# Optimization experiments

Hardware: AMD Instinct MI355X
Metric: run time of the kernel (lower is better)

## Reference

```python
import jax, jax.numpy as jnp
import numpy as np

B, T, D, H = 32, 512, 1024, 1024


def setup_inputs() -> dict:
    key = jax.random.key(0)
    k1, k2, k3 = jax.random.split(key, 3)
    x = jax.random.normal(k1, (B, T, D), dtype=jnp.float32)
    c0 = jnp.zeros((B, H), dtype=jnp.float32)
    h0 = jnp.zeros((B, H), dtype=jnp.float32)
    # scale weights so gates do not saturate
    Wx = jax.random.normal(k2, (D, 4 * H), dtype=jnp.float32) * 0.05
    Wh = jax.random.normal(k3, (H, 4 * H), dtype=jnp.float32) * 0.05
    b = jnp.zeros((4 * H,), dtype=jnp.float32)
    return {"x": x, "c0": c0, "h0": h0, "Wx": Wx, "Wh": Wh, "b": b}


def reference(x, c0, h0, Wx, Wh, b):
    # Flax LSTMCell: gates = x @ Wx + h @ Wh + b, split into i,f,g,o.
    # Precompute the input projection for all timesteps (one big GEMM).
    xW = jnp.einsum('btd,dg->btg', x, Wx) + b  # [B,T,4H]

    def step(carry, xw_t):
        c, h = carry
        gates = xw_t + h @ Wh  # [B,4H]
        i, f, g, o = jnp.split(gates, 4, axis=-1)
        i = jax.nn.sigmoid(i)
        f = jax.nn.sigmoid(f)
        g = jnp.tanh(g)
        o = jax.nn.sigmoid(o)
        c_new = f * c + i * g
        h_new = o * jnp.tanh(c_new)
        return (c_new, h_new), h_new

    (cT, hT), ys = jax.lax.scan(step, (c0, h0), jnp.swapaxes(xW, 0, 1))
    outputs = jnp.swapaxes(ys, 0, 1)  # [B,T,H]
    return outputs, (cT, hT)
```

## Files before the change

kernel.cpp:

```cpp
#include <hip/hip_runtime.h>
#include <cstddef>

#define NB 32
#define NT 512
#define ND 1024
#define NH 1024
#define NG 4096
#define GRID 256

typedef unsigned short ushortT;
typedef __attribute__((ext_vector_type(8))) short short8;
typedef __attribute__((ext_vector_type(4))) float f32x4;
typedef __attribute__((ext_vector_type(4))) unsigned uint4v;

#define GLL16(g, l) __builtin_amdgcn_global_load_lds(                      \
    (const __attribute__((address_space(1))) void*)(g),                    \
    (__attribute__((address_space(3))) void*)(l), 16, 0, 0)

__device__ __forceinline__ ushortT f2bf(float f) {
    union { float f; unsigned u; } v; v.f = f;
    unsigned r = v.u + 0x7FFFu + ((v.u >> 16) & 1u);
    return (ushortT)(r >> 16);
}
__device__ __forceinline__ float bf2f(ushortT u) {
    union { unsigned u; float f; } v; v.u = (unsigned)u << 16; return v.f;
}

__device__ __forceinline__ float pick4(float a0, float a1, float a2, float a3, int s) {
    float lo = (s & 1) ? a1 : a0;
    float hi = (s & 1) ? a3 : a2;
    return (s & 2) ? hi : lo;
}

__device__ __forceinline__ float fsigmoid(float x) {
    return __builtin_amdgcn_rcpf(1.f + __expf(-x));
}
__device__ __forceinline__ float ftanh(float x) {
    float xc = fminf(fmaxf(x, -15.f), 15.f);
    float e  = __expf(-2.f * xc);
    return (1.f - e) * __builtin_amdgcn_rcpf(1.f + e);
}

__global__ __launch_bounds__(256) void cast_bf16(const float* __restrict__ src,
                                                 ushortT* __restrict__ dst, int n4)
{
    int i = blockIdx.x * 256 + threadIdx.x;
    if (i < n4) {
        float4 v = ((const float4*)src)[i];
        ushort4 o;
        o.x = f2bf(v.x); o.y = f2bf(v.y); o.z = f2bf(v.z); o.w = f2bf(v.w);
        ((ushort4*)dst)[i] = o;
    }
}

__global__ __launch_bounds__(256) void transpose_cast(
    const float* __restrict__ src, ushortT* __restrict__ dst, int permute)
{
    __shared__ ushortT tile[64][66];
    const int c0 = blockIdx.x * 64, r0 = blockIdx.y * 64;
    const int cc = threadIdx.x & 63, rq = threadIdx.x >> 6;
    #pragma unroll
    for (int ps = 0; ps < 16; ++ps) {
        int r = ps * 4 + rq;
        tile[cc][r] = f2bf(src[(size_t)(r0 + r) * NG + c0 + cc]);
    }
    __syncthreads();
    #pragma unroll
    for (int ps = 0; ps < 16; ++ps) {
        int cl = ps * 4 + rq;
        int n  = c0 + cl;
        int drow = permute ? ((((n & 1023) >> 2) << 4) | ((n >> 10) << 2) | (n & 3))
                           : n;
        dst[(size_t)drow * 1024 + r0 + cc] = tile[cl][cc];
    }
}

__global__ __launch_bounds__(256) void gemm_xw_mfma(
    const ushortT* __restrict__ xb,
    const ushortT* __restrict__ wxT,
    const float* __restrict__ bias,
    ushortT* __restrict__ XWPb,
    int t0, int Tc, int tcsh)
{
    __shared__ ushortT As[128 * 32];
    __shared__ ushortT Bs[128 * 32];

    const int tid  = threadIdx.x;
    const int lane = tid & 63;
    const int wv   = tid >> 6;
    const int wr   = wv >> 1, wc = wv & 1;
    const int n0   = blockIdx.x * 128;
    const int m0   = blockIdx.y * 128;

    const int c1 = tid, c2 = tid + 256;
    const int rm1 = m0 + (c1 >> 2), rm2 = m0 + (c2 >> 2);
    const int xr1 = ((rm1 >> tcsh) * NT) + t0 + (rm1 & (Tc - 1));
    const int xr2 = ((rm2 >> tcsh) * NT) + t0 + (rm2 & (Tc - 1));
    const ushortT* ap1 = xb + (size_t)xr1 * ND + (c1 & 3) * 8;
    const ushortT* ap2 = xb + (size_t)xr2 * ND + (c2 & 3) * 8;
    const ushortT* bp1 = wxT + (size_t)(n0 + (c1 >> 2)) * ND + (c1 & 3) * 8;
    const ushortT* bp2 = wxT + (size_t)(n0 + (c2 >> 2)) * ND + (c2 & 3) * 8;

    f32x4 acc[4][4];
    #pragma unroll
    for (int m = 0; m < 4; ++m)
        #pragma unroll
        for (int n = 0; n < 4; ++n) acc[m][n] = (f32x4){0.f, 0.f, 0.f, 0.f};

    const int arow_base = (wr * 64 + (lane & 15)) * 32 + (lane >> 4) * 8;
    const int brow_base = (wc * 64 + (lane & 15)) * 32 + (lane >> 4) * 8;

    for (int k0 = 0; k0 < ND; k0 += 32) {
        __syncthreads();
        GLL16(ap1 + k0, &As[c1 * 8]);
        GLL16(ap2 + k0, &As[c2 * 8]);
        GLL16(bp1 + k0, &Bs[c1 * 8]);
        GLL16(bp2 + k0, &Bs[c2 * 8]);
        __syncthreads();
        short8 af[4], bf[4];
        #pragma unroll
        for (int m = 0; m < 4; ++m)
            af[m] = *(const short8*)&As[arow_base + m * 16 * 32];
        #pragma unroll
        for (int n = 0; n < 4; ++n)
            bf[n] = *(const short8*)&Bs[brow_base + n * 16 * 32];
        #pragma unroll
        for (int m = 0; m < 4; ++m)
            #pragma unroll
            for (int n = 0; n < 4; ++n)
                acc[m][n] = __builtin_amdgcn_mfma_f32_16x16x32_bf16(
                    af[m], bf[n], acc[m][n], 0, 0, 0);
    }

    #pragma unroll
    for (int n = 0; n < 4; ++n) {
        int col = n0 + wc * 64 + n * 16 + (lane & 15);
        int pc  = (((col & 1023) >> 2) << 4) | ((col >> 10) << 2) | (col & 3);
        float bs = bias[col];
        #pragma unroll
        for (int m = 0; m < 4; ++m) {
            #pragma unroll
            for (int r = 0; r < 4; ++r) {
                int rm = m0 + wr * 64 + m * 16 + (lane >> 4) * 4 + r;
                int b  = rm >> tcsh, tr = rm & (Tc - 1);
                XWPb[((size_t)tr * NB + b) * NG + pc] = f2bf(acc[m][n][r] + bs);
            }
        }
    }
}

__global__ __launch_bounds__(512) void lstm_persist(
    const ushortT* __restrict__ XWPb,
    const ushortT* __restrict__ whpT,
    ushortT* __restrict__ hbuf,
    const float* __restrict__ cinit,
    float* __restrict__ cT,
    float* __restrict__ out,
    float* __restrict__ hT,
    unsigned* __restrict__ flags,
    int t0, int Tc)
{
    __shared__ float red[2][64][16][4];

    const int tid  = threadIdx.x;
    const int lane = tid & 63;
    const int w    = tid >> 6;
    const int grp  = blockIdx.x & 7;
    const int sl   = blockIdx.x >> 3;

    const int lo = lane & 15;
    const int hi = lane >> 4;

    short8 Bf[8][4];
    #pragma unroll
    for (int ct = 0; ct < 8; ++ct)
        #pragma unroll
        for (int ks = 0; ks < 4; ++ks)
            Bf[ct][ks] = *(const short8*)(whpT
                + (size_t)(sl * 128 + ct * 16 + lo) * NH + w * 128 + ks * 32 + hi * 8);

    const int arow = tid >> 7;
    const int acol = tid & 127;
    const int gq   = (acol >> 2) & 3;
    const int u4   = (acol >> 4) * 4 + (acol & 3);
    const int brow = grp * 4 + arow;
    const int j    = sl * 32 + u4;

    float creg = cinit[(size_t)brow * NH + j];

    const int aoff = (grp * 4 + (lane & 3)) * NH + w * 128 + hi * 8;

    unsigned* const fg = flags + grp * 32;
    unsigned* const fpoll = fg + 4 * w + (lane & 3);
    unsigned* const fmine = fg + sl;

    ushortT xvr = XWPb[(size_t)brow * NG + sl * 128 + acol];

    const int tend = t0 + Tc;
    for (int t = t0; t < tend; ++t) {
        const int trel = t - t0;
        const int par  = t & 1;
        const ushortT* hRp = hbuf + (size_t)par * (NB * NH);
        ushortT*       hWp = hbuf + (size_t)(par ^ 1) * (NB * NH);

        if (trel) {
            const unsigned tgt = (unsigned)trel;
            for (int it = 0; it < (1 << 17); ++it) {
                unsigned v = __hip_atomic_load(fpoll, __ATOMIC_RELAXED,
                                               __HIP_MEMORY_SCOPE_AGENT);
                if (__all(v >= tgt)) break;
            }
        }

        const unsigned long long* sp = (const unsigned long long*)(hRp + aoff);
        unsigned long long p0, p1;
        uint4v Araw0, Araw1, Araw2, Araw3;
        p0 = __hip_atomic_load(sp + 0, __ATOMIC_RELAXED, __HIP_MEMORY_SCOPE_AGENT);
        p1 = __hip_atomic_load(sp + 1, __ATOMIC_RELAXED, __HIP_MEMORY_SCOPE_AGENT);
        Araw0 = (uint4v){(unsigned)p0, (unsigned)(p0 >> 32), (unsigned)p1, (unsigned)(p1 >> 32)};
        p0 = __hip_atomic_load(sp + 8, __ATOMIC_RELAXED, __HIP_MEMORY_SCOPE_AGENT);
        p1 = __hip_atomic_load(sp + 9, __ATOMIC_RELAXED, __HIP_MEMORY_SCOPE_AGENT);
        Araw1 = (uint4v){(unsigned)p0, (unsigned)(p0 >> 32), (unsigned)p1, (unsigned)(p1 >> 32)};
        p0 = __hip_atomic_load(sp + 16, __ATOMIC_RELAXED, __HIP_MEMORY_SCOPE_AGENT);
        p1 = __hip_atomic_load(sp + 17, __ATOMIC_RELAXED, __HIP_MEMORY_SCOPE_AGENT);
        Araw2 = (uint4v){(unsigned)p0, (unsigned)(p0 >> 32), (unsigned)p1, (unsigned)(p1 >> 32)};
        p0 = __hip_atomic_load(sp + 24, __ATOMIC_RELAXED, __HIP_MEMORY_SCOPE_AGENT);
        p1 = __hip_atomic_load(sp + 25, __ATOMIC_RELAXED, __HIP_MEMORY_SCOPE_AGENT);
        Araw3 = (uint4v){(unsigned)p0, (unsigned)(p0 >> 32), (unsigned)p1, (unsigned)(p1 >> 32)};

        short8 A0 = *(short8*)&Araw0;
        short8 A1 = *(short8*)&Araw1;
        short8 A2 = *(short8*)&Araw2;
        short8 A3 = *(short8*)&Araw3;

        #pragma unroll
        for (int ct = 0; ct < 8; ++ct) {
            f32x4 a = (f32x4){0.f, 0.f, 0.f, 0.f};
            a = __builtin_amdgcn_mfma_f32_16x16x32_bf16(A0, Bf[ct][0], a, 0, 0, 0);
            a = __builtin_amdgcn_mfma_f32_16x16x32_bf16(A1, Bf[ct][1], a, 0, 0, 0);
            a = __builtin_amdgcn_mfma_f32_16x16x32_bf16(A2, Bf[ct][2], a, 0, 0, 0);
            a = __builtin_amdgcn_mfma_f32_16x16x32_bf16(A3, Bf[ct][3], a, 0, 0, 0);
            if (hi == 0)
                *(f32x4*)&red[par][w * 8 + ct][lo][0] = a;
        }
        __syncthreads();

        float g = bf2f(xvr);
        #pragma unroll
        for (int wv = 0; wv < 8; ++wv)
            g += red[par][wv * 8 + (acol >> 4)][acol & 15][arow];

        float g4  = __shfl_xor(g, 4);
        float g8  = __shfl_xor(g, 8);
        float g12 = __shfl_xor(g, 12);

        float gi = pick4(g, g4, g8, g12, gq);
        float gf = pick4(g, g4, g8, g12, gq ^ 1);
        float gg = pick4(g, g4, g8, g12, gq ^ 2);
        float go = pick4(g, g4, g8, g12, gq ^ 3);

        float iv = fsigmoid(gi);
        float fv = fsigmoid(gf);
        float gv = ftanh(gg);
        float ov = fsigmoid(go);
        float cn = fv * creg + iv * gv;
        float hn = ov * ftanh(cn);
        creg = cn;

        float ph = __shfl_xor(hn, 1);
        const bool wl = (gq == 0) && ((acol & 1) == 0);
        unsigned pair = (unsigned)f2bf(hn) | ((unsigned)f2bf(ph) << 16);
        unsigned* hdst = (unsigned*)(hWp + (size_t)brow * NH + (j & ~1));
        if (wl)
            __hip_atomic_store(hdst, pair, __ATOMIC_RELAXED,
                               __HIP_MEMORY_SCOPE_AGENT);

        asm volatile("s_waitcnt vmcnt(0)" ::: "memory");
        __syncthreads();

        if (t != tend - 1) {
            if (tid == 0)
                __hip_atomic_store(fmine, (unsigned)(trel + 1),
                                   __ATOMIC_RELAXED, __HIP_MEMORY_SCOPE_AGENT);
            if (wl)
                *(float2*)&out[((size_t)brow * NT + t) * NH + j] = make_float2(hn, ph);
            xvr = XWPb[((size_t)(trel + 1) * NB + brow) * NG + sl * 128 + acol];
        } else {
            if (wl)
                *(float2*)&out[((size_t)brow * NT + t) * NH + j] = make_float2(hn, ph);
            if (gq == 0) {
                if (t == NT - 1) hT[(size_t)brow * NH + j] = hn;
                cT[(size_t)brow * NH + j] = cn;
            }
        }
    }
}

extern "C" void kernel_launch(void* const* d_in, const int* in_sizes, int n_in,
                              void* d_out, int out_size, void* d_ws, size_t ws_size,
                              hipStream_t stream) {
    const float* x    = (const float*)d_in[0];
    const float* c0   = (const float*)d_in[1];
    const float* h0   = (const float*)d_in[2];
    const float* Wx   = (const float*)d_in[3];
    const float* Wh   = (const float*)d_in[4];
    const float* bias = (const float*)d_in[5];

    float* out = (float*)d_out;
    float* cT  = out + (size_t)NB * NT * NH;
    float* hT  = cT + (size_t)NB * NH;

    ushortT* xb   = (ushortT*)d_ws;
    ushortT* wxT  = xb  + (size_t)NB * NT * ND;
    ushortT* whpT = wxT + (size_t)NG * ND;
    ushortT* hbuf = whpT + (size_t)NG * NH;
    unsigned* flags = (unsigned*)(hbuf + 2 * NB * NH);
    ushortT* xwpb = (ushortT*)(flags + 8 * 32 + 32);

    const size_t fixed = ((size_t)NB * NT * ND + (size_t)NG * ND + (size_t)NG * NH
                          + 2 * NB * NH) * sizeof(ushortT)
                         + (8 * 32 + 32) * sizeof(unsigned) + 256;
    int Tc = 512;
    while (Tc > 4 && fixed + (size_t)NB * Tc * NG * sizeof(ushortT) > ws_size)
        Tc >>= 1;
    int tcsh = 31 - __builtin_clz(Tc);

    cast_bf16<<<(NB * NT * ND / 4 + 255) / 256, 256, 0, stream>>>(x, xb, NB * NT * ND / 4);
    cast_bf16<<<(NB * NH / 4 + 255) / 256, 256, 0, stream>>>(h0, hbuf, NB * NH / 4);
    transpose_cast<<<dim3(64, 16), 256, 0, stream>>>(Wx, wxT, 0);
    transpose_cast<<<dim3(64, 16), 256, 0, stream>>>(Wh, whpT, 1);

    for (int t0 = 0; t0 < NT; t0 += Tc) {
        dim3 g(NG / 128, (NB * Tc) / 128);
        gemm_xw_mfma<<<g, 256, 0, stream>>>(xb, wxT, bias, xwpb, t0, Tc, tcsh);
        hipMemsetAsync(flags, 0, (8 * 32) * sizeof(unsigned), stream);
        lstm_persist<<<GRID, 512, 0, stream>>>(
            xwpb, whpT, hbuf,
            (t0 == 0) ? c0 : (const float*)cT,
            cT, out, hT, flags, t0, Tc);
    }
}
```

Measured before the change: 2.370 ms.

## Replace per-block flag barrier with step-tagged h words polled directly

Each bf16 pair of h is now stored as a 64-bit word whose upper half carries the timestep tag. Consumers spin on the data words themselves instead of on separate per-block flags. This removes the flag store, the vmcnt wait and the trailing __syncthreads per step, so one global round trip leaves the critical path. In exchange the hidden-state buffer and each poll's traffic double, since 16 u64 atomic loads replace 8. Correctness relies on tags differing between reuses of the double buffer, including across chunk launches.

```diff
diff --git a/kernel.cpp b/kernel.cpp
--- a/kernel.cpp
+++ b/kernel.cpp
@@ -9,6 +9,7 @@
 #define GRID 256
 
 typedef unsigned short ushortT;
+typedef unsigned long long u64;
 typedef __attribute__((ext_vector_type(8))) short short8;
 typedef __attribute__((ext_vector_type(4))) float f32x4;
 typedef __attribute__((ext_vector_type(4))) unsigned uint4v;
@@ -51,6 +52,16 @@
         o.x = f2bf(v.x); o.y = f2bf(v.y); o.z = f2bf(v.z); o.w = f2bf(v.w);
         ((ushort4*)dst)[i] = o;
     }
+}
+
+__global__ __launch_bounds__(256) void cast_h0_tagged(
+    const float* __restrict__ h0, u64* __restrict__ dst)
+{
+    int i = blockIdx.x * 256 + threadIdx.x;
+    int row = i >> 9, p = i & 511;
+    unsigned pair = (unsigned)f2bf(h0[(size_t)row * NH + 2 * p])
+                  | ((unsigned)f2bf(h0[(size_t)row * NH + 2 * p + 1]) << 16);
+    dst[i] = (u64)pair;
 }
 
 __global__ __launch_bounds__(256) void transpose_cast(
@@ -152,12 +163,11 @@
 __global__ __launch_bounds__(512) void lstm_persist(
     const ushortT* __restrict__ XWPb,
     const ushortT* __restrict__ whpT,
-    ushortT* __restrict__ hbuf,
+    u64* __restrict__ hbuf64,
     const float* __restrict__ cinit,
     float* __restrict__ cT,
     float* __restrict__ out,
     float* __restrict__ hT,
-    unsigned* __restrict__ flags,
     int t0, int Tc)
 {
     __shared__ float red[2][64][16][4];
@@ -188,11 +198,9 @@
 
     float creg = cinit[(size_t)brow * NH + j];
 
-    const int aoff = (grp * 4 + (lane & 3)) * NH + w * 128 + hi * 8;
-
-    unsigned* const fg = flags + grp * 32;
-    unsigned* const fpoll = fg + 4 * w + (lane & 3);
-    unsigned* const fmine = fg + sl;
+    const int prow = grp * 4 + (lane & 3);
+    const size_t pbase = (size_t)prow * 512 + w * 64 + hi * 4;
+    const size_t wbase = (size_t)brow * 512 + sl * 16 + (u4 >> 1);
 
     ushortT xvr = XWPb[(size_t)brow * NG + sl * 128 + acol];
 
@@ -200,38 +208,46 @@
     for (int t = t0; t < tend; ++t) {
         const int trel = t - t0;
         const int par  = t & 1;
-        const ushortT* hRp = hbuf + (size_t)par * (NB * NH);
-        ushortT*       hWp = hbuf + (size_t)(par ^ 1) * (NB * NH);
-
-        if (trel) {
-            const unsigned tgt = (unsigned)trel;
-            for (int it = 0; it < (1 << 17); ++it) {
-                unsigned v = __hip_atomic_load(fpoll, __ATOMIC_RELAXED,
-                                               __HIP_MEMORY_SCOPE_AGENT);
-                if (__all(v >= tgt)) break;
-            }
-        }
-
-        const unsigned long long* sp = (const unsigned long long*)(hRp + aoff);
-        unsigned long long p0, p1;
-        uint4v Araw0, Araw1, Araw2, Araw3;
-        p0 = __hip_atomic_load(sp + 0, __ATOMIC_RELAXED, __HIP_MEMORY_SCOPE_AGENT);
-        p1 = __hip_atomic_load(sp + 1, __ATOMIC_RELAXED, __HIP_MEMORY_SCOPE_AGENT);
-        Araw0 = (uint4v){(unsigned)p0, (unsigned)(p0 >> 32), (unsigned)p1, (unsigned)(p1 >> 32)};
-        p0 = __hip_atomic_load(sp + 8, __ATOMIC_RELAXED, __HIP_MEMORY_SCOPE_AGENT);
-        p1 = __hip_atomic_load(sp + 9, __ATOMIC_RELAXED, __HIP_MEMORY_SCOPE_AGENT);
-        Araw1 = (uint4v){(unsigned)p0, (unsigned)(p0 >> 32), (unsigned)p1, (unsigned)(p1 >> 32)};
-        p0 = __hip_atomic_load(sp + 16, __ATOMIC_RELAXED, __HIP_MEMORY_SCOPE_AGENT);
-        p1 = __hip_atomic_load(sp + 17, __ATOMIC_RELAXED, __HIP_MEMORY_SCOPE_AGENT);
-        Araw2 = (uint4v){(unsigned)p0, (unsigned)(p0 >> 32), (unsigned)p1, (unsigned)(p1 >> 32)};
-        p0 = __hip_atomic_load(sp + 24, __ATOMIC_RELAXED, __HIP_MEMORY_SCOPE_AGENT);
-        p1 = __hip_atomic_load(sp + 25, __ATOMIC_RELAXED, __HIP_MEMORY_SCOPE_AGENT);
-        Araw3 = (uint4v){(unsigned)p0, (unsigned)(p0 >> 32), (unsigned)p1, (unsigned)(p1 >> 32)};
-
-        short8 A0 = *(short8*)&Araw0;
-        short8 A1 = *(short8*)&Araw1;
-        short8 A2 = *(short8*)&Araw2;
-        short8 A3 = *(short8*)&Araw3;
+
+        const u64* rp = hbuf64 + (size_t)par * 16384 + pbase;
+        u64 v0, v1, v2, v3, v4, v5, v6, v7, v8, v9, va, vb, vc, vd, ve, vf;
+        const unsigned tgt = (unsigned)t;
+        for (int it = 0; it < (1 << 17); ++it) {
+            v0 = __hip_atomic_load(rp + 0,  __ATOMIC_RELAXED, __HIP_MEMORY_SCOPE_AGENT);
+            v1 = __hip_atomic_load(rp + 1,  __ATOMIC_RELAXED, __HIP_MEMORY_SCOPE_AGENT);
+            v2 = __hip_atomic_load(rp + 2,  __ATOMIC_RELAXED, __HIP_MEMORY_SCOPE_AGENT);
+            v3 = __hip_atomic_load(rp + 3,  __ATOMIC_RELAXED, __HIP_MEMORY_SCOPE_AGENT);
+            v4 = __hip_atomic_load(rp + 16, __ATOMIC_RELAXED, __HIP_MEMORY_SCOPE_AGENT);
+            v5 = __hip_atomic_load(rp + 17, __ATOMIC_RELAXED, __HIP_MEMORY_SCOPE_AGENT);
+            v6 = __hip_atomic_load(rp + 18, __ATOMIC_RELAXED, __HIP_MEMORY_SCOPE_AGENT);
+            v7 = __hip_atomic_load(rp + 19, __ATOMIC_RELAXED, __HIP_MEMORY_SCOPE_AGENT);
+            v8 = __hip_atomic_load(rp + 32, __ATOMIC_RELAXED, __HIP_MEMORY_SCOPE_AGENT);
+            v9 = __hip_atomic_load(rp + 33, __ATOMIC_RELAXED, __HIP_MEMORY_SCOPE_AGENT);
+            va = __hip_atomic_load(rp + 34, __ATOMIC_RELAXED, __HIP_MEMORY_SCOPE_AGENT);
+            vb = __hip_atomic_load(rp + 35, __ATOMIC_RELAXED, __HIP_MEMORY_SCOPE_AGENT);
+            vc = __hip_atomic_load(rp + 48, __ATOMIC_RELAXED, __HIP_MEMORY_SCOPE_AGENT);
+            vd = __hip_atomic_load(rp + 49, __ATOMIC_RELAXED, __HIP_MEMORY_SCOPE_AGENT);
+            ve = __hip_atomic_load(rp + 50, __ATOMIC_RELAXED, __HIP_MEMORY_SCOPE_AGENT);
+            vf = __hip_atomic_load(rp + 51, __ATOMIC_RELAXED, __HIP_MEMORY_SCOPE_AGENT);
+            bool ok = ((unsigned)(v0 >> 32) == tgt) & ((unsigned)(v1 >> 32) == tgt)
+                    & ((unsigned)(v2 >> 32) == tgt) & ((unsigned)(v3 >> 32) == tgt)
+                    & ((unsigned)(v4 >> 32) == tgt) & ((unsigned)(v5 >> 32) == tgt)
+                    & ((unsigned)(v6 >> 32) == tgt) & ((unsigned)(v7 >> 32) == tgt)
+                    & ((unsigned)(v8 >> 32) == tgt) & ((unsigned)(v9 >> 32) == tgt)
+                    & ((unsigned)(va >> 32) == tgt) & ((unsigned)(vb >> 32) == tgt)
+                    & ((unsigned)(vc >> 32) == tgt) & ((unsigned)(vd >> 32) == tgt)
+                    & ((unsigned)(ve >> 32) == tgt) & ((unsigned)(vf >> 32) == tgt);
+            if (__all(ok)) break;
+        }
+
+        uint4v d0 = (uint4v){(unsigned)v0, (unsigned)v1, (unsigned)v2, (unsigned)v3};
+        uint4v d1 = (uint4v){(unsigned)v4, (unsigned)v5, (unsigned)v6, (unsigned)v7};
+        uint4v d2 = (uint4v){(unsigned)v8, (unsigned)v9, (unsigned)va, (unsigned)vb};
+        uint4v d3 = (uint4v){(unsigned)vc, (unsigned)vd, (unsigned)ve, (unsigned)vf};
+        short8 A0 = *(short8*)&d0;
+        short8 A1 = *(short8*)&d1;
+        short8 A2 = *(short8*)&d2;
+        short8 A3 = *(short8*)&d3;
 
         #pragma unroll
         for (int ct = 0; ct < 8; ++ct) {
@@ -269,25 +285,18 @@
 
         float ph = __shfl_xor(hn, 1);
         const bool wl = (gq == 0) && ((acol & 1) == 0);
-        unsigned pair = (unsigned)f2bf(hn) | ((unsigned)f2bf(ph) << 16);
-        unsigned* hdst = (unsigned*)(hWp + (size_t)brow * NH + (j & ~1));
+        if (wl) {
+            unsigned pair = (unsigned)f2bf(hn) | ((unsigned)f2bf(ph) << 16);
+            u64 word = (u64)pair | ((u64)(unsigned)(t + 1) << 32);
+            __hip_atomic_store(hbuf64 + (size_t)(par ^ 1) * 16384 + wbase, word,
+                               __ATOMIC_RELAXED, __HIP_MEMORY_SCOPE_AGENT);
+        }
+
         if (wl)
-            __hip_atomic_store(hdst, pair, __ATOMIC_RELAXED,
-                               __HIP_MEMORY_SCOPE_AGENT);
-
-        asm volatile("s_waitcnt vmcnt(0)" ::: "memory");
-        __syncthreads();
-
+            *(float2*)&out[((size_t)brow * NT + t) * NH + j] = make_float2(hn, ph);
         if (t != tend - 1) {
-            if (tid == 0)
-                __hip_atomic_store(fmine, (unsigned)(trel + 1),
-                                   __ATOMIC_RELAXED, __HIP_MEMORY_SCOPE_AGENT);
-            if (wl)
-                *(float2*)&out[((size_t)brow * NT + t) * NH + j] = make_float2(hn, ph);
             xvr = XWPb[((size_t)(trel + 1) * NB + brow) * NG + sl * 128 + acol];
         } else {
-            if (wl)
-                *(float2*)&out[((size_t)brow * NT + t) * NH + j] = make_float2(hn, ph);
             if (gq == 0) {
                 if (t == NT - 1) hT[(size_t)brow * NH + j] = hn;
                 cT[(size_t)brow * NH + j] = cn;
@@ -313,30 +322,28 @@
     ushortT* xb   = (ushortT*)d_ws;
     ushortT* wxT  = xb  + (size_t)NB * NT * ND;
     ushortT* whpT = wxT + (size_t)NG * ND;
-    ushortT* hbuf = whpT + (size_t)NG * NH;
-    unsigned* flags = (unsigned*)(hbuf + 2 * NB * NH);
-    ushortT* xwpb = (ushortT*)(flags + 8 * 32 + 32);
+    u64*     hbuf64 = (u64*)(whpT + (size_t)NG * NH);
+    ushortT* xwpb = (ushortT*)(hbuf64 + 2 * 32 * 512);
 
     const size_t fixed = ((size_t)NB * NT * ND + (size_t)NG * ND + (size_t)NG * NH
-                          + 2 * NB * NH) * sizeof(ushortT)
-                         + (8 * 32 + 32) * sizeof(unsigned) + 256;
+                          + 0) * sizeof(ushortT) + 2 * 32 * 512 * 8 + 256;
     int Tc = 512;
     while (Tc > 4 && fixed + (size_t)NB * Tc * NG * sizeof(ushortT) > ws_size)
         Tc >>= 1;
     int tcsh = 31 - __builtin_clz(Tc);
 
     cast_bf16<<<(NB * NT * ND / 4 + 255) / 256, 256, 0, stream>>>(x, xb, NB * NT * ND / 4);
-    cast_bf16<<<(NB * NH / 4 + 255) / 256, 256, 0, stream>>>(h0, hbuf, NB * NH / 4);
+    cast_h0_tagged<<<64, 256, 0, stream>>>(h0, hbuf64);
+    hipMemsetAsync(hbuf64 + 16384, 0, 16384 * sizeof(u64), stream);
     transpose_cast<<<dim3(64, 16), 256, 0, stream>>>(Wx, wxT, 0);
     transpose_cast<<<dim3(64, 16), 256, 0, stream>>>(Wh, whpT, 1);
 
     for (int t0 = 0; t0 < NT; t0 += Tc) {
         dim3 g(NG / 128, (NB * Tc) / 128);
         gemm_xw_mfma<<<g, 256, 0, stream>>>(xb, wxT, bias, xwpb, t0, Tc, tcsh);
-        hipMemsetAsync(flags, 0, (8 * 32) * sizeof(unsigned), stream);
         lstm_persist<<<GRID, 512, 0, stream>>>(
-            xwpb, whpT, hbuf,
+            xwpb, whpT, hbuf64,
             (t0 == 0) ? c0 : (const float*)cT,
-            cT, out, hT, flags, t0, Tc);
-    }
-}
+            cT, out, hT, t0, Tc);
+    }
+}
```

After: 3.114 ms. 31.4% more time.
